# Kernel optimization log

Hardware: AMD Instinct MI355X
Metric: run time of the kernel (lower is better)

Reference implementation:

```python
import jax, jax.numpy as jnp
import numpy as np

B, L, D, H, DK = 2, 1024, 1024, 16, 64
LN_EPS = 1e-5


def setup_inputs() -> dict:
    key = jax.random.key(0)
    ks = jax.random.split(key, 4)
    x = jax.random.normal(ks[0], (B, L, D), dtype=jnp.float32)
    W_qkv = jax.random.normal(ks[1], (D, 3 * D), dtype=jnp.float32) * 0.02
    W_o = jax.random.normal(ks[2], (D, D), dtype=jnp.float32) * 0.02
    W_LTM = jax.random.normal(ks[3], (H, DK, DK), dtype=jnp.float32) * 0.5
    return {
        "x": x,
        "W_qkv": W_qkv,
        "W_o": W_o,
        "W_LTM": W_LTM,
        "V_gs": jnp.zeros((H,), jnp.float32),
        "V_T0": jnp.zeros((H,), jnp.float32),
        "beta_tau": jnp.ones((H,), jnp.float32),
        "beta_gm": jnp.ones((H,), jnp.float32) * 0.1,
        "C_ch": jnp.ones((H,), jnp.float32),
        "gamma": jnp.ones((H,), jnp.float32) * 0.1,
        "alpha_ppd": jnp.ones((1,), jnp.float32),
        "IC_threshold": jnp.ones((1,), jnp.float32),
        "gate": jnp.zeros((H,), jnp.float32),
    }


def _stp_physics(W_LTM, V_gs, V_T0, beta_tau, beta_gm, C_ch, alpha_ppd, IC_threshold):
    # per-head params broadcast to (H, dk, dk)
    V_eff = V_gs[:, None, None] - V_T0[:, None, None] + W_LTM  # U_T = 1.0
    sp = jax.nn.softplus(V_eff)
    g_ch = beta_tau[:, None, None] * sp
    retention = jnp.exp(-g_ch / C_ch[:, None, None])  # = 1 - Lambda
    G = beta_gm[:, None, None] * sp * jax.nn.sigmoid(V_eff)
    sign_mask = jnp.tanh(alpha_ppd * (g_ch - IC_threshold))
    return retention, G, sign_mask


def reference(x, W_qkv, W_o, W_LTM, V_gs, V_T0, beta_tau, beta_gm, C_ch,
              gamma, alpha_ppd, IC_threshold, gate):
    Bb, Ll, Dd = x.shape
    qkv = (x @ W_qkv).reshape(Bb, Ll, 3, H, DK)
    q, k, v = qkv[:, :, 0], qkv[:, :, 1], qkv[:, :, 2]  # (B,L,H,dk)

    # LayerNorm over dk, no affine
    mu = jnp.mean(k, axis=-1, keepdims=True)
    var = jnp.var(k, axis=-1, keepdims=True)
    k_normed = (k - mu) * jax.lax.rsqrt(var + LN_EPS)

    # ---- causal softmax attention ----
    scale = 1.0 / np.sqrt(DK)
    attn = jnp.einsum('bihd,bjhd->bhij', q, k) * scale
    causal = jnp.tril(jnp.ones((Ll, Ll), dtype=bool))
    attn = jnp.where(causal[None, None], attn, -jnp.inf)
    attn = jax.nn.softmax(attn, axis=-1)
    softmax_out = jnp.einsum('bhij,bjhd->bihd', attn, v)  # (B,L,H,dk)

    # ---- STP fast-weight recurrence ----
    retention, G, sign_mask = _stp_physics(W_LTM, V_gs, V_T0, beta_tau,
                                           beta_gm, C_ch, alpha_ppd, IC_threshold)
    coeff = gamma[:, None, None] * sign_mask * G  # (H,dk,dk)

    def step(F_state, qkv_t):
        q_t, k_t, v_t = qkv_t  # (B,H,dk) each; k_t is normed
        hebbian = jnp.einsum('bhd,bhe->bhde', v_t, k_t)
        F_new = retention[None] * F_state + coeff[None] * hebbian
        y_t = jnp.einsum('bhde,bhe->bhd', W_LTM[None] + F_new, q_t)
        return F_new, y_t

    xs = (jnp.moveaxis(q, 1, 0), jnp.moveaxis(k_normed, 1, 0), jnp.moveaxis(v, 1, 0))
    F0 = jnp.zeros((Bb, H, DK, DK), dtype=x.dtype)
    _, ys = jax.lax.scan(step, F0, xs)
    stp_out = jnp.moveaxis(ys, 0, 1)  # (B,L,H,dk)

    g = jax.nn.sigmoid(gate)[None, None, :, None]
    y = g * softmax_out + (1.0 - g) * stp_out
    y = y.reshape(Bb, Ll, Dd)
    return y @ W_o
```

## Files before the change

### kernel.cpp

```cpp
#include <hip/hip_runtime.h>
#include <hip/hip_bf16.h>
#include <math.h>

#define LQ 1024
#define DH 1024
#define NH 16
#define DKH 64

typedef __bf16 bf16x8 __attribute__((ext_vector_type(8)));
typedef float f32x4 __attribute__((ext_vector_type(4)));
typedef const unsigned int __attribute__((address_space(1)))* gas1_t;
typedef unsigned int __attribute__((address_space(3)))* las3_t;

__device__ __forceinline__ unsigned pack2bf(float a, float b) {
  union { __hip_bfloat16 h[2]; unsigned u; } t;
  t.h[0] = __float2bfloat16(a);
  t.h[1] = __float2bfloat16(b);
  return t.u;
}
__device__ __forceinline__ void store_c(float* p, float v) { *p = v; }
__device__ __forceinline__ void store_c(__hip_bfloat16* p, float v) { *p = __float2bfloat16(v); }
__device__ __forceinline__ void bf4w(float* dst, uint2 r) {
  dst[0] = __uint_as_float(r.x << 16);
  dst[1] = __uint_as_float(r.x & 0xffff0000u);
  dst[2] = __uint_as_float(r.y << 16);
  dst[3] = __uint_as_float(r.y & 0xffff0000u);
}

__global__ __launch_bounds__(256) void prep_kernel(
    const float* __restrict__ x, const float* __restrict__ W_qkv, const float* __restrict__ W_o,
    const float* __restrict__ W_LTM, const float* __restrict__ V_gs, const float* __restrict__ V_T0,
    const float* __restrict__ beta_tau, const float* __restrict__ beta_gm, const float* __restrict__ C_ch,
    const float* __restrict__ gamma_, const float* __restrict__ alpha_ppd, const float* __restrict__ IC_thr,
    const float* __restrict__ gate,
    __hip_bfloat16* __restrict__ xb, __hip_bfloat16* __restrict__ wqt, __hip_bfloat16* __restrict__ wot,
    float* __restrict__ ret, float* __restrict__ ret64, float* __restrict__ co, float* __restrict__ g_out) {
  __shared__ float ts[32][33];
  const int bx = blockIdx.x, tid = threadIdx.x;
  if (bx < 256) {
    int idx = bx * 256 + tid;
    int h = idx >> 12;
    float w = W_LTM[idx];
    float veff = V_gs[h] - V_T0[h] + w;
    float sp = fmaxf(veff, 0.f) + log1pf(expf(-fabsf(veff)));
    float gch = beta_tau[h] * sp;
    float e1 = gch / C_ch[h];
    float sig = 1.f / (1.f + expf(-veff));
    float G = beta_gm[h] * sp * sig;
    float sm = tanhf(alpha_ppd[0] * (gch - IC_thr[0]));
    ret[idx] = expf(-e1);
    ret64[idx] = expf(-64.f * e1);
    co[idx] = gamma_[h] * sm * G;
    if (idx < NH) g_out[idx] = 1.f / (1.f + expf(-gate[idx]));
  } else if (bx < 2304) {
    size_t i = (size_t)((bx - 256) * 256 + tid) * 4;
    float4 v = *(const float4*)(x + i);
    __hip_bfloat16 t[4] = {__float2bfloat16(v.x), __float2bfloat16(v.y),
                           __float2bfloat16(v.z), __float2bfloat16(v.w)};
    *(uint2*)(xb + i) = *(uint2*)t;
  } else {
    const float* W;
    __hip_bfloat16* Wt;
    int n0, k0, N;
    if (bx < 5376) {
      int idx = bx - 2304;
      W = W_qkv; Wt = wqt; N = 3072;
      n0 = (idx % 96) * 32; k0 = (idx / 96) * 32;
    } else {
      int idx = bx - 5376;
      W = W_o; Wt = wot; N = 1024;
      n0 = (idx & 31) * 32; k0 = (idx >> 5) * 32;
    }
    int r = tid >> 5, c = tid & 31;
#pragma unroll
    for (int i = 0; i < 4; i++) ts[r + 8 * i][c] = W[(size_t)(k0 + r + 8 * i) * N + n0 + c];
    __syncthreads();
#pragma unroll
    for (int i = 0; i < 4; i++)
      Wt[(size_t)(n0 + r + 8 * i) * 1024 + k0 + c] = __float2bfloat16(ts[c][r + 8 * i]);
  }
}

template <typename OT>
__global__ __launch_bounds__(256) void gemm_bt_kernel(
    const __hip_bfloat16* __restrict__ A, const __hip_bfloat16* __restrict__ Bt,
    OT* __restrict__ C, int M, int N, int K) {
  __shared__ unsigned short As[128 * 32];
  __shared__ unsigned short Bs[128 * 32];
  const int tid = threadIdx.x;
  const int w = tid >> 6, lane = tid & 63;
  const int quad = lane >> 4, l16 = lane & 15;
  const int wm = w & 1, wn = w >> 1;
  const int row0 = blockIdx.y * 128, col0 = blockIdx.x * 128;
  const int sr = lane >> 2;
  const int sk = (lane & 3) * 8;
  f32x4 acc[4][4];
#pragma unroll
  for (int i = 0; i < 4; i++)
#pragma unroll
    for (int j = 0; j < 4; j++) acc[i][j] = (f32x4){0.f, 0.f, 0.f, 0.f};

  for (int k0 = 0; k0 < K; k0 += 32) {
    __syncthreads();
#pragma unroll
    for (int c = 0; c < 2; c++) {
      int s = c * 4 + w;
      const __hip_bfloat16* gA = A + (size_t)(row0 + s * 16 + sr) * K + k0 + sk;
      __builtin_amdgcn_global_load_lds((gas1_t)gA, (las3_t)((char*)As + s * 1024), 16, 0, 0);
      const __hip_bfloat16* gB = Bt + (size_t)(col0 + s * 16 + sr) * K + k0 + sk;
      __builtin_amdgcn_global_load_lds((gas1_t)gB, (las3_t)((char*)Bs + s * 1024), 16, 0, 0);
    }
    __syncthreads();
    bf16x8 af[4], bfr[4];
#pragma unroll
    for (int i = 0; i < 4; i++)
      af[i] = *(const bf16x8*)((const char*)As + (((wm * 64 + i * 16 + l16) * 32 + quad * 8) << 1));
#pragma unroll
    for (int j = 0; j < 4; j++)
      bfr[j] = *(const bf16x8*)((const char*)Bs + (((wn * 64 + j * 16 + l16) * 32 + quad * 8) << 1));
#pragma unroll
    for (int i = 0; i < 4; i++)
#pragma unroll
      for (int j = 0; j < 4; j++)
        acc[i][j] = __builtin_amdgcn_mfma_f32_16x16x32_bf16(af[i], bfr[j], acc[i][j], 0, 0, 0);
  }
#pragma unroll
  for (int i = 0; i < 4; i++) {
    int rowb = row0 + wm * 64 + i * 16 + quad * 4;
#pragma unroll
    for (int j = 0; j < 4; j++) {
      int col = col0 + wn * 64 + j * 16 + l16;
#pragma unroll
      for (int r = 0; r < 4; r++)
        store_c(&C[(size_t)(rowb + r) * N + col], acc[i][j][r]);
    }
  }
}

__global__ __launch_bounds__(256) void cvt_qkv_kernel(
    const __hip_bfloat16* __restrict__ qkvb, __hip_bfloat16* __restrict__ vt,
    __hip_bfloat16* __restrict__ knb) {
  const int tc = blockIdx.x, h = blockIdx.y, b = blockIdx.z;
  const int bh = b * NH + h;
  const int tid = threadIdx.x;
  const int r = tid >> 2;
  const int q4 = tid & 3;
  const int t = tc * 64 + r;
  __shared__ float Ls[64][65];
  const size_t rowbase = (size_t)(b * LQ + t) * 3 * DH + h * DKH + q4 * 16;

  {
    bf16x8 k0 = *(const bf16x8*)(qkvb + rowbase + DH);
    bf16x8 k1 = *(const bf16x8*)(qkvb + rowbase + DH + 8);
    float vv[16];
#pragma unroll
    for (int i = 0; i < 8; i++) { vv[i] = (float)k0[i]; vv[8 + i] = (float)k1[i]; }
    float s1 = 0.f, s2 = 0.f;
#pragma unroll
    for (int i = 0; i < 16; i++) { s1 += vv[i]; s2 += vv[i] * vv[i]; }
    s1 += __shfl_xor(s1, 1); s2 += __shfl_xor(s2, 1);
    s1 += __shfl_xor(s1, 2); s2 += __shfl_xor(s2, 2);
    float mu = s1 * (1.f / 64.f);
    float var = s2 * (1.f / 64.f) - mu * mu;
    float inv = rsqrtf(var + 1e-5f);
    __hip_bfloat16 ko[16];
#pragma unroll
    for (int i = 0; i < 16; i++) ko[i] = __float2bfloat16((vv[i] - mu) * inv);
    __hip_bfloat16* kdst = knb + ((size_t)(b * LQ + t) * NH + h) * DKH + q4 * 16;
    *(uint4*)kdst = *(uint4*)ko;
    *(uint4*)(kdst + 8) = *(uint4*)(ko + 8);
  }
  {
    bf16x8 v0 = *(const bf16x8*)(qkvb + rowbase + 2 * DH);
    bf16x8 v1 = *(const bf16x8*)(qkvb + rowbase + 2 * DH + 8);
#pragma unroll
    for (int i = 0; i < 8; i++) {
      Ls[r][q4 * 16 + i] = (float)v0[i];
      Ls[r][q4 * 16 + 8 + i] = (float)v1[i];
    }
  }
  __syncthreads();
  {
    const int dr = tid >> 2, tq = tid & 3;
    __hip_bfloat16 o[16];
#pragma unroll
    for (int i = 0; i < 16; i++) o[i] = __float2bfloat16(Ls[tq * 16 + i][dr]);
    __hip_bfloat16* dst = vt + ((size_t)bh * DKH + dr) * LQ + tc * 64 + tq * 16;
    *(uint4*)dst = *(uint4*)o;
    *(uint4*)(dst + 8) = *(uint4*)(o + 8);
  }
}

__global__ __launch_bounds__(256) void attn_mfma_kernel(
    const __hip_bfloat16* __restrict__ qkvb, const __hip_bfloat16* __restrict__ vt,
    __hip_bfloat16* __restrict__ sob) {
  const int it = 15 - blockIdx.x;
  const int h = blockIdx.y, b = blockIdx.z;
  const int bh = b * NH + h;
  const int tid = threadIdx.x;
  const int w = tid >> 6, lane = tid & 63;
  const int l16 = lane & 15, quad = lane >> 4;
  __shared__ __attribute__((aligned(16))) __hip_bfloat16 Ks[8 * 64 * 8];
  __shared__ __attribute__((aligned(16))) __hip_bfloat16 Vs[8 * 64 * 8];
  const int i0 = it * 64;
  const int q_abs = i0 + w * 16 + l16;
  bf16x8 aq[2];
  aq[0] = *(const bf16x8*)(qkvb + (size_t)(b * LQ + q_abs) * 3 * DH + h * DKH + quad * 8);
  aq[1] = *(const bf16x8*)(qkvb + (size_t)(b * LQ + q_abs) * 3 * DH + h * DKH + 32 + quad * 8);
  f32x4 o[4];
#pragma unroll
  for (int dt = 0; dt < 4; dt++) o[dt] = (f32x4){0.f, 0.f, 0.f, 0.f};
  float mrun = -3e38f, lrun = 0.f;

  for (int jt = 0; jt <= it; jt++) {
    const int j0 = jt * 64;
    __syncthreads();
#pragma unroll
    for (int ff = 0; ff < 2; ff++) {
      const int f = w * 2 + ff;
      const int nt = f >> 1, kk = f & 1;
      const __hip_bfloat16* gk = qkvb + (size_t)(b * LQ + j0 + nt * 16 + l16) * 3 * DH + DH +
                                 h * DKH + kk * 32 + quad * 8;
      __builtin_amdgcn_global_load_lds((gas1_t)gk, (las3_t)(Ks + f * 512), 16, 0, 0);
      const __hip_bfloat16* gv = vt + ((size_t)bh * DKH + nt * 16 + l16) * LQ + j0 + kk * 32 + quad * 8;
      __builtin_amdgcn_global_load_lds((gas1_t)gv, (las3_t)(Vs + f * 512), 16, 0, 0);
    }
    __syncthreads();
    f32x4 s[4];
#pragma unroll
    for (int nt = 0; nt < 4; nt++) s[nt] = (f32x4){0.f, 0.f, 0.f, 0.f};
#pragma unroll
    for (int kk = 0; kk < 2; kk++)
#pragma unroll
      for (int nt = 0; nt < 4; nt++) {
        bf16x8 bk = *(const bf16x8*)(Ks + ((nt * 2 + kk) * 64 + lane) * 8);
        s[nt] = __builtin_amdgcn_mfma_f32_16x16x32_bf16(bk, aq[kk], s[nt], 0, 0, 0);
      }
#pragma unroll
    for (int nt = 0; nt < 4; nt++)
#pragma unroll
      for (int r = 0; r < 4; r++) {
        float sv = s[nt][r] * 0.125f;
        if (jt == it && (j0 + nt * 16 + quad * 4 + r > q_abs)) sv = -1e30f;
        s[nt][r] = sv;
      }
    float mx = -3e38f;
#pragma unroll
    for (int nt = 0; nt < 4; nt++)
#pragma unroll
      for (int r = 0; r < 4; r++) mx = fmaxf(mx, s[nt][r]);
    mx = fmaxf(mx, __shfl_xor(mx, 16));
    mx = fmaxf(mx, __shfl_xor(mx, 32));
    float mn = fmaxf(mrun, mx);
    float al = __expf(mrun - mn);
    mrun = mn;
    float p[4][4];
    float rs = 0.f;
#pragma unroll
    for (int nt = 0; nt < 4; nt++)
#pragma unroll
      for (int r = 0; r < 4; r++) {
        float pv = __expf(s[nt][r] - mn);
        p[nt][r] = pv;
        rs += pv;
      }
    rs += __shfl_xor(rs, 16);
    rs += __shfl_xor(rs, 32);
    lrun = lrun * al + rs;
    unsigned pk[4][2];
#pragma unroll
    for (int nt = 0; nt < 4; nt++) {
      pk[nt][0] = pack2bf(p[nt][0], p[nt][1]);
      pk[nt][1] = pack2bf(p[nt][2], p[nt][3]);
    }
    const int srcA = l16 | ((quad & 1) << 5);
    const bool hi_sel = (quad >> 1) != 0;
    bf16x8 ap[2];
#pragma unroll
    for (int kk = 0; kk < 2; kk++) {
      union { unsigned u[4]; bf16x8 v; } cv;
#pragma unroll
      for (int g = 0; g < 2; g++) {
        int src = srcA + (g << 4);
        unsigned lo0 = (unsigned)__shfl((int)pk[kk * 2][0], src);
        unsigned lo1 = (unsigned)__shfl((int)pk[kk * 2][1], src);
        unsigned hi0 = (unsigned)__shfl((int)pk[kk * 2 + 1][0], src);
        unsigned hi1 = (unsigned)__shfl((int)pk[kk * 2 + 1][1], src);
        cv.u[g * 2] = hi_sel ? hi0 : lo0;
        cv.u[g * 2 + 1] = hi_sel ? hi1 : lo1;
      }
      ap[kk] = cv.v;
    }
#pragma unroll
    for (int dt = 0; dt < 4; dt++)
#pragma unroll
      for (int r = 0; r < 4; r++) o[dt][r] *= al;
#pragma unroll
    for (int kk = 0; kk < 2; kk++)
#pragma unroll
      for (int dt = 0; dt < 4; dt++) {
        bf16x8 bv = *(const bf16x8*)(Vs + ((dt * 2 + kk) * 64 + lane) * 8);
        o[dt] = __builtin_amdgcn_mfma_f32_16x16x32_bf16(bv, ap[kk], o[dt], 0, 0, 0);
      }
  }
  float inv = 1.f / lrun;
  __hip_bfloat16* ob = sob + ((size_t)(b * LQ + q_abs) * NH + h) * DKH + quad * 4;
#pragma unroll
  for (int dt = 0; dt < 4; dt++) {
    uint2 val = {pack2bf(o[dt][0] * inv, o[dt][1] * inv),
                 pack2bf(o[dt][2] * inv, o[dt][3] * inv)};
    *(uint2*)(ob + dt * 16) = val;
  }
}

__global__ __launch_bounds__(256) void state_kernel(
    const __hip_bfloat16* __restrict__ qkvb, const __hip_bfloat16* __restrict__ knb,
    const float* __restrict__ ret_g, const float* __restrict__ co_g, float* __restrict__ S) {
  const int bh = blockIdx.x >> 1;
  const int half = blockIdx.x & 1;
  const int c = blockIdx.y;
  const int bb = bh >> 4, h = bh & 15;
  const int tid = threadIdx.x;
  const int dl = tid >> 3, j = tid & 7;
  const int d = half * 32 + dl;
  float F[8], R[8], Cc[8];
  const int base = h * 4096 + d * 64 + j * 8;
#pragma unroll
  for (int i = 0; i < 8; i++) {
    F[i] = 0.f;
    R[i] = ret_g[base + i];
    Cc[i] = co_g[base + i];
  }
  __shared__ float kb[2][8][64], vb[2][8][64];
  const int t00 = c * 64;
  const int sten = tid >> 7;
  const int sli = tid & 127;
  const int ss = sli >> 4;
  const int se = (sli & 15) * 4;
  {
    int t = t00 + ss;
    uint2 raw = (sten == 0)
        ? *(const uint2*)(knb + ((size_t)(bb * LQ + t) * NH + h) * DKH + se)
        : *(const uint2*)(qkvb + ((size_t)(bb * LQ + t) * 3 + 2) * DH + h * DKH + se);
    bf4w(sten == 0 ? &kb[0][ss][se] : &vb[0][ss][se], raw);
  }
  __syncthreads();
  for (int sc = 0; sc < 8; sc++) {
    const int p = sc & 1;
    uint2 raw;
    if (sc < 7) {
      int t = t00 + (sc + 1) * 8 + ss;
      raw = (sten == 0)
          ? *(const uint2*)(knb + ((size_t)(bb * LQ + t) * NH + h) * DKH + se)
          : *(const uint2*)(qkvb + ((size_t)(bb * LQ + t) * 3 + 2) * DH + h * DKH + se);
    }
#pragma unroll
    for (int s = 0; s < 8; s++) {
      float vd = vb[p][s][d];
      float4 k0 = *(const float4*)&kb[p][s][j * 8];
      float4 k1 = *(const float4*)&kb[p][s][j * 8 + 4];
      float ke[8] = {k0.x, k0.y, k0.z, k0.w, k1.x, k1.y, k1.z, k1.w};
#pragma unroll
      for (int i = 0; i < 8; i++) F[i] = fmaf(Cc[i] * vd, ke[i], R[i] * F[i]);
    }
    if (sc < 7) bf4w(sten == 0 ? &kb[p ^ 1][ss][se] : &vb[p ^ 1][ss][se], raw);
    __syncthreads();
  }
  const size_t sb = ((size_t)c * 2048 + ((size_t)bb * 16 + h) * 64 + d) * 64 + j * 8;
#pragma unroll
  for (int i = 0; i < 8; i++) S[sb + i] = F[i];
}

__global__ __launch_bounds__(256) void combine_kernel(
    const float* __restrict__ S, const float* __restrict__ ret64, float* __restrict__ Fs) {
  int n = blockIdx.x * 256 + threadIdx.x;
  float r64 = ret64[n & 65535];
  float F = 0.f;
  Fs[n] = 0.f;
#pragma unroll
  for (int c = 1; c < 16; c++) {
    F = fmaf(r64, F, S[(size_t)(c - 1) * 131072 + n]);
    Fs[(size_t)c * 131072 + n] = F;
  }
}

__global__ __launch_bounds__(256) void scan_out_kernel(
    const __hip_bfloat16* __restrict__ qkvb, const __hip_bfloat16* __restrict__ knb,
    const float* __restrict__ W_LTM, const float* __restrict__ ret_g, const float* __restrict__ co_g,
    const float* __restrict__ Fs, const __hip_bfloat16* __restrict__ sob,
    const float* __restrict__ g, __hip_bfloat16* __restrict__ mixb) {
  const int bh = blockIdx.x >> 1;
  const int half = blockIdx.x & 1;
  const int c = blockIdx.y;
  const int bb = bh >> 4, h = bh & 15;
  const int tid = threadIdx.x;
  const int dl = tid >> 3, j = tid & 7;
  const int d = half * 32 + dl;
  const float gh = g[h];
  float F[8], R[8], Cc[8], W[8];
  const int base = h * 4096 + d * 64 + j * 8;
  const size_t nbase = (size_t)c * 131072 + (((size_t)bb * 16 + h) * 64 + d) * 64 + j * 8;
#pragma unroll
  for (int i = 0; i < 8; i++) {
    F[i] = Fs[nbase + i];
    R[i] = ret_g[base + i];
    Cc[i] = co_g[base + i];
    W[i] = W_LTM[base + i];
  }
  __shared__ float qb[2][8][64], kb[2][8][64], vb[2][8][64];
  const int t00 = c * 64;
  const int sten = tid >> 7;
  const int sli = tid & 127;
  const int ss = sli >> 4;
  const int se = (sli & 15) * 4;
  const int vs = tid >> 5;
  const int ve = (tid & 31) * 2;
  {
    int t = t00 + ss, tv = t00 + vs;
    uint2 rqk = (sten == 0)
        ? *(const uint2*)(qkvb + (size_t)(bb * LQ + t) * 3 * DH + h * DKH + se)
        : *(const uint2*)(knb + ((size_t)(bb * LQ + t) * NH + h) * DKH + se);
    unsigned rv = *(const unsigned*)(qkvb + ((size_t)(bb * LQ + tv) * 3 + 2) * DH + h * DKH + ve);
    bf4w(sten == 0 ? &qb[0][ss][se] : &kb[0][ss][se], rqk);
    vb[0][vs][ve] = __uint_as_float(rv << 16);
    vb[0][vs][ve + 1] = __uint_as_float(rv & 0xffff0000u);
  }
  __syncthreads();
  for (int sc = 0; sc < 8; sc++) {
    const int p = sc & 1;
    uint2 rqk;
    unsigned rv;
    if (sc < 7) {
      int t = t00 + (sc + 1) * 8 + ss, tv = t00 + (sc + 1) * 8 + vs;
      rqk = (sten == 0)
          ? *(const uint2*)(qkvb + (size_t)(bb * LQ + t) * 3 * DH + h * DKH + se)
          : *(const uint2*)(knb + ((size_t)(bb * LQ + t) * NH + h) * DKH + se);
      rv = *(const unsigned*)(qkvb + ((size_t)(bb * LQ + tv) * 3 + 2) * DH + h * DKH + ve);
    }
    float ykeep = 0.f;
#pragma unroll
    for (int s = 0; s < 8; s++) {
      float vd = vb[p][s][d];
      float4 k0 = *(const float4*)&kb[p][s][j * 8];
      float4 k1 = *(const float4*)&kb[p][s][j * 8 + 4];
      float4 q0 = *(const float4*)&qb[p][s][j * 8];
      float4 q1 = *(const float4*)&qb[p][s][j * 8 + 4];
      float ke[8] = {k0.x, k0.y, k0.z, k0.w, k1.x, k1.y, k1.z, k1.w};
      float qe[8] = {q0.x, q0.y, q0.z, q0.w, q1.x, q1.y, q1.z, q1.w};
      float yp = 0.f;
#pragma unroll
      for (int i = 0; i < 8; i++) {
        F[i] = fmaf(Cc[i] * vd, ke[i], R[i] * F[i]);
        yp = fmaf(W[i] + F[i], qe[i], yp);
      }
      yp += __shfl_xor(yp, 1);
      yp += __shfl_xor(yp, 2);
      yp += __shfl_xor(yp, 4);
      if (j == s) ykeep = yp;
    }
    {
      const size_t oi = ((size_t)(bb * LQ + t00 + sc * 8 + j) * NH + h) * DKH + d;
      float sv = __bfloat162float(sob[oi]);
      mixb[oi] = __float2bfloat16(gh * sv + (1.f - gh) * ykeep);
    }
    if (sc < 7) {
      bf4w(sten == 0 ? &qb[p ^ 1][ss][se] : &kb[p ^ 1][ss][se], rqk);
      vb[p ^ 1][vs][ve] = __uint_as_float(rv << 16);
      vb[p ^ 1][vs][ve + 1] = __uint_as_float(rv & 0xffff0000u);
    }
    __syncthreads();
  }
}

extern "C" void kernel_launch(void* const* d_in, const int* in_sizes, int n_in,
                              void* d_out, int out_size, void* d_ws, size_t ws_size,
                              hipStream_t stream) {
  (void)in_sizes; (void)n_in; (void)out_size; (void)ws_size;
  const float* x        = (const float*)d_in[0];
  const float* W_qkv    = (const float*)d_in[1];
  const float* W_o      = (const float*)d_in[2];
  const float* W_LTM    = (const float*)d_in[3];
  const float* V_gs     = (const float*)d_in[4];
  const float* V_T0     = (const float*)d_in[5];
  const float* beta_tau = (const float*)d_in[6];
  const float* beta_gm  = (const float*)d_in[7];
  const float* C_ch     = (const float*)d_in[8];
  const float* gamma_   = (const float*)d_in[9];
  const float* alpha_p  = (const float*)d_in[10];
  const float* IC_thr   = (const float*)d_in[11];
  const float* gate     = (const float*)d_in[12];

  float* ws  = (float*)d_ws;
  __hip_bfloat16* qkvb = (__hip_bfloat16*)ws;
  __hip_bfloat16* knb  = (__hip_bfloat16*)(ws + 3145728);
  __hip_bfloat16* sob  = (__hip_bfloat16*)(ws + 4194304);
  __hip_bfloat16* mixb = (__hip_bfloat16*)(ws + 5242880);
  __hip_bfloat16* vtb  = (__hip_bfloat16*)(ws + 6291456);
  __hip_bfloat16* xb   = (__hip_bfloat16*)(ws + 7340032);
  __hip_bfloat16* wqt  = (__hip_bfloat16*)(ws + 8388608);
  __hip_bfloat16* wot  = (__hip_bfloat16*)(ws + 9961472);
  float* ret   = ws + 10485760;
  float* ret64 = ret + 65536;
  float* co    = ret64 + 65536;
  float* g     = co + 65536;
  float* Sbuf  = g + 64;
  float* Fs    = Sbuf + 1966080;
  float* out = (float*)d_out;

  prep_kernel<<<6400, 256, 0, stream>>>(x, W_qkv, W_o, W_LTM, V_gs, V_T0, beta_tau, beta_gm,
                                        C_ch, gamma_, alpha_p, IC_thr, gate,
                                        xb, wqt, wot, ret, ret64, co, g);
  gemm_bt_kernel<__hip_bfloat16><<<dim3(24, 16), 256, 0, stream>>>(xb, wqt, qkvb, 2048, 3072, 1024);
  cvt_qkv_kernel<<<dim3(16, 16, 2), 256, 0, stream>>>(qkvb, vtb, knb);
  attn_mfma_kernel<<<dim3(16, 16, 2), 256, 0, stream>>>(qkvb, vtb, sob);
  state_kernel<<<dim3(64, 15), 256, 0, stream>>>(qkvb, knb, ret, co, Sbuf);
  combine_kernel<<<512, 256, 0, stream>>>(Sbuf, ret64, Fs);
  scan_out_kernel<<<dim3(64, 16), 256, 0, stream>>>(qkvb, knb, W_LTM, ret, co, Fs, sob, g, mixb);
  gemm_bt_kernel<float><<<dim3(8, 16), 256, 0, stream>>>(mixb, wot, out, 2048, 1024, 1024);
}
```

Baseline: 218.0 us.

## Fuse K layernorm and V transpose into QKV GEMM epilogue; smaller output GEMM tiles

The separate cvt_qkv kernel is removed. The QKV GEMM epilogue now computes the per-head LayerNorm of K from accumulator registers using cross-lane shuffles, and writes the transposed V through an LDS buffer that is unioned with the GEMM tiles. This saves a kernel launch and a re-read of the K and V sections from global memory, at the cost of extra epilogue work in two thirds of the blocks. Separately, the output projection uses a new 64x64-tile GEMM with 512 blocks instead of 128, to fill more compute units at the cost of less data reuse per block.

```diff
diff --git a/kernel.cpp b/kernel.cpp
--- a/kernel.cpp
+++ b/kernel.cpp
@@ -18,8 +18,10 @@
   t.h[1] = __float2bfloat16(b);
   return t.u;
 }
-__device__ __forceinline__ void store_c(float* p, float v) { *p = v; }
-__device__ __forceinline__ void store_c(__hip_bfloat16* p, float v) { *p = __float2bfloat16(v); }
+__device__ __forceinline__ unsigned short bfbits(float x) {
+  __hip_bfloat16 h = __float2bfloat16(x);
+  return *(unsigned short*)&h;
+}
 __device__ __forceinline__ void bf4w(float* dst, uint2 r) {
   dst[0] = __uint_as_float(r.x << 16);
   dst[1] = __uint_as_float(r.x & 0xffff0000u);
@@ -81,12 +83,14 @@
   }
 }
 
-template <typename OT>
-__global__ __launch_bounds__(256) void gemm_bt_kernel(
+__global__ __launch_bounds__(256) void gemm_qkv_kernel(
     const __hip_bfloat16* __restrict__ A, const __hip_bfloat16* __restrict__ Bt,
-    OT* __restrict__ C, int M, int N, int K) {
-  __shared__ unsigned short As[128 * 32];
-  __shared__ unsigned short Bs[128 * 32];
+    __hip_bfloat16* __restrict__ C, __hip_bfloat16* __restrict__ knb,
+    __hip_bfloat16* __restrict__ vt, int M, int N, int K) {
+  __shared__ union {
+    struct { unsigned short As[128 * 32]; unsigned short Bs[128 * 32]; } ab;
+    unsigned short Vt[4][64][68];
+  } sm;
   const int tid = threadIdx.x;
   const int w = tid >> 6, lane = tid & 63;
   const int quad = lane >> 4, l16 = lane & 15;
@@ -106,18 +110,18 @@
     for (int c = 0; c < 2; c++) {
       int s = c * 4 + w;
       const __hip_bfloat16* gA = A + (size_t)(row0 + s * 16 + sr) * K + k0 + sk;
-      __builtin_amdgcn_global_load_lds((gas1_t)gA, (las3_t)((char*)As + s * 1024), 16, 0, 0);
+      __builtin_amdgcn_global_load_lds((gas1_t)gA, (las3_t)((char*)sm.ab.As + s * 1024), 16, 0, 0);
       const __hip_bfloat16* gB = Bt + (size_t)(col0 + s * 16 + sr) * K + k0 + sk;
-      __builtin_amdgcn_global_load_lds((gas1_t)gB, (las3_t)((char*)Bs + s * 1024), 16, 0, 0);
+      __builtin_amdgcn_global_load_lds((gas1_t)gB, (las3_t)((char*)sm.ab.Bs + s * 1024), 16, 0, 0);
     }
     __syncthreads();
     bf16x8 af[4], bfr[4];
 #pragma unroll
     for (int i = 0; i < 4; i++)
-      af[i] = *(const bf16x8*)((const char*)As + (((wm * 64 + i * 16 + l16) * 32 + quad * 8) << 1));
+      af[i] = *(const bf16x8*)((const char*)sm.ab.As + (((wm * 64 + i * 16 + l16) * 32 + quad * 8) << 1));
 #pragma unroll
     for (int j = 0; j < 4; j++)
-      bfr[j] = *(const bf16x8*)((const char*)Bs + (((wn * 64 + j * 16 + l16) * 32 + quad * 8) << 1));
+      bfr[j] = *(const bf16x8*)((const char*)sm.ab.Bs + (((wn * 64 + j * 16 + l16) * 32 + quad * 8) << 1));
 #pragma unroll
     for (int i = 0; i < 4; i++)
 #pragma unroll
@@ -132,62 +136,113 @@
       int col = col0 + wn * 64 + j * 16 + l16;
 #pragma unroll
       for (int r = 0; r < 4; r++)
-        store_c(&C[(size_t)(rowb + r) * N + col], acc[i][j][r]);
-    }
-  }
-}
-
-__global__ __launch_bounds__(256) void cvt_qkv_kernel(
-    const __hip_bfloat16* __restrict__ qkvb, __hip_bfloat16* __restrict__ vt,
-    __hip_bfloat16* __restrict__ knb) {
-  const int tc = blockIdx.x, h = blockIdx.y, b = blockIdx.z;
-  const int bh = b * NH + h;
+        C[(size_t)(rowb + r) * N + col] = __float2bfloat16(acc[i][j][r]);
+    }
+  }
+  const int sec = col0 >> 10;
+  if (sec == 1) {
+    const int hh = ((col0 & 1023) >> 6) + wn;
+#pragma unroll
+    for (int i = 0; i < 4; i++) {
+      f32x4 s1 = {0.f, 0.f, 0.f, 0.f}, s2 = {0.f, 0.f, 0.f, 0.f};
+#pragma unroll
+      for (int j = 0; j < 4; j++)
+#pragma unroll
+        for (int r = 0; r < 4; r++) {
+          s1[r] += acc[i][j][r];
+          s2[r] += acc[i][j][r] * acc[i][j][r];
+        }
+#pragma unroll
+      for (int m = 1; m <= 8; m <<= 1)
+#pragma unroll
+        for (int r = 0; r < 4; r++) {
+          s1[r] += __shfl_xor(s1[r], m);
+          s2[r] += __shfl_xor(s2[r], m);
+        }
+#pragma unroll
+      for (int r = 0; r < 4; r++) {
+        float mu = s1[r] * (1.f / 64.f);
+        float var = s2[r] * (1.f / 64.f) - mu * mu;
+        float inv = rsqrtf(var + 1e-5f);
+        int row = row0 + wm * 64 + i * 16 + quad * 4 + r;
+#pragma unroll
+        for (int j = 0; j < 4; j++)
+          knb[((size_t)row * NH + hh) * DKH + j * 16 + l16] = __float2bfloat16((acc[i][j][r] - mu) * inv);
+      }
+    }
+  } else if (sec == 2) {
+    __syncthreads();
+    const int hh = ((col0 & 1023) >> 6) + wn;
+#pragma unroll
+    for (int i = 0; i < 4; i++)
+#pragma unroll
+      for (int j = 0; j < 4; j++)
+#pragma unroll
+        for (int r = 0; r < 4; r++)
+          sm.Vt[w][j * 16 + l16][i * 16 + quad * 4 + r] = bfbits(acc[i][j][r]);
+    const int b = row0 >> 10;
+    const int t0 = (row0 & 1023) + wm * 64;
+    const int bh = b * NH + hh;
+    const int cc = lane & 7, ddl = lane >> 3;
+#pragma unroll
+    for (int pass = 0; pass < 8; pass++) {
+      int d = pass * 8 + ddl;
+      uint2 a0 = *(const uint2*)&sm.Vt[w][d][cc * 8];
+      uint2 a1 = *(const uint2*)&sm.Vt[w][d][cc * 8 + 4];
+      uint4 val = {a0.x, a0.y, a1.x, a1.y};
+      *(uint4*)(vt + ((size_t)bh * DKH + d) * LQ + t0 + cc * 8) = val;
+    }
+  }
+}
+
+__global__ __launch_bounds__(256) void gemm_bt64_kernel(
+    const __hip_bfloat16* __restrict__ A, const __hip_bfloat16* __restrict__ Bt,
+    float* __restrict__ C, int M, int N, int K) {
+  __shared__ unsigned short As[64 * 32];
+  __shared__ unsigned short Bs[64 * 32];
   const int tid = threadIdx.x;
-  const int r = tid >> 2;
-  const int q4 = tid & 3;
-  const int t = tc * 64 + r;
-  __shared__ float Ls[64][65];
-  const size_t rowbase = (size_t)(b * LQ + t) * 3 * DH + h * DKH + q4 * 16;
-
-  {
-    bf16x8 k0 = *(const bf16x8*)(qkvb + rowbase + DH);
-    bf16x8 k1 = *(const bf16x8*)(qkvb + rowbase + DH + 8);
-    float vv[16];
-#pragma unroll
-    for (int i = 0; i < 8; i++) { vv[i] = (float)k0[i]; vv[8 + i] = (float)k1[i]; }
-    float s1 = 0.f, s2 = 0.f;
-#pragma unroll
-    for (int i = 0; i < 16; i++) { s1 += vv[i]; s2 += vv[i] * vv[i]; }
-    s1 += __shfl_xor(s1, 1); s2 += __shfl_xor(s2, 1);
-    s1 += __shfl_xor(s1, 2); s2 += __shfl_xor(s2, 2);
-    float mu = s1 * (1.f / 64.f);
-    float var = s2 * (1.f / 64.f) - mu * mu;
-    float inv = rsqrtf(var + 1e-5f);
-    __hip_bfloat16 ko[16];
-#pragma unroll
-    for (int i = 0; i < 16; i++) ko[i] = __float2bfloat16((vv[i] - mu) * inv);
-    __hip_bfloat16* kdst = knb + ((size_t)(b * LQ + t) * NH + h) * DKH + q4 * 16;
-    *(uint4*)kdst = *(uint4*)ko;
-    *(uint4*)(kdst + 8) = *(uint4*)(ko + 8);
-  }
-  {
-    bf16x8 v0 = *(const bf16x8*)(qkvb + rowbase + 2 * DH);
-    bf16x8 v1 = *(const bf16x8*)(qkvb + rowbase + 2 * DH + 8);
-#pragma unroll
-    for (int i = 0; i < 8; i++) {
-      Ls[r][q4 * 16 + i] = (float)v0[i];
-      Ls[r][q4 * 16 + 8 + i] = (float)v1[i];
-    }
-  }
-  __syncthreads();
-  {
-    const int dr = tid >> 2, tq = tid & 3;
-    __hip_bfloat16 o[16];
-#pragma unroll
-    for (int i = 0; i < 16; i++) o[i] = __float2bfloat16(Ls[tq * 16 + i][dr]);
-    __hip_bfloat16* dst = vt + ((size_t)bh * DKH + dr) * LQ + tc * 64 + tq * 16;
-    *(uint4*)dst = *(uint4*)o;
-    *(uint4*)(dst + 8) = *(uint4*)(o + 8);
+  const int w = tid >> 6, lane = tid & 63;
+  const int quad = lane >> 4, l16 = lane & 15;
+  const int wm = w & 1, wn = w >> 1;
+  const int row0 = blockIdx.y * 64, col0 = blockIdx.x * 64;
+  const int sr = lane >> 2;
+  const int sk = (lane & 3) * 8;
+  f32x4 acc[2][2];
+#pragma unroll
+  for (int i = 0; i < 2; i++)
+#pragma unroll
+    for (int j = 0; j < 2; j++) acc[i][j] = (f32x4){0.f, 0.f, 0.f, 0.f};
+
+  for (int k0 = 0; k0 < K; k0 += 32) {
+    __syncthreads();
+    const __hip_bfloat16* gA = A + (size_t)(row0 + w * 16 + sr) * K + k0 + sk;
+    __builtin_amdgcn_global_load_lds((gas1_t)gA, (las3_t)((char*)As + w * 1024), 16, 0, 0);
+    const __hip_bfloat16* gB = Bt + (size_t)(col0 + w * 16 + sr) * K + k0 + sk;
+    __builtin_amdgcn_global_load_lds((gas1_t)gB, (las3_t)((char*)Bs + w * 1024), 16, 0, 0);
+    __syncthreads();
+    bf16x8 af[2], bfr[2];
+#pragma unroll
+    for (int i = 0; i < 2; i++)
+      af[i] = *(const bf16x8*)((const char*)As + (((wm * 32 + i * 16 + l16) * 32 + quad * 8) << 1));
+#pragma unroll
+    for (int j = 0; j < 2; j++)
+      bfr[j] = *(const bf16x8*)((const char*)Bs + (((wn * 32 + j * 16 + l16) * 32 + quad * 8) << 1));
+#pragma unroll
+    for (int i = 0; i < 2; i++)
+#pragma unroll
+      for (int j = 0; j < 2; j++)
+        acc[i][j] = __builtin_amdgcn_mfma_f32_16x16x32_bf16(af[i], bfr[j], acc[i][j], 0, 0, 0);
+  }
+#pragma unroll
+  for (int i = 0; i < 2; i++) {
+    int rowb = row0 + wm * 32 + i * 16 + quad * 4;
+#pragma unroll
+    for (int j = 0; j < 2; j++) {
+      int col = col0 + wn * 32 + j * 16 + l16;
+#pragma unroll
+      for (int r = 0; r < 4; r++)
+        C[(size_t)(rowb + r) * N + col] = acc[i][j][r];
+    }
   }
 }
 
@@ -510,11 +565,10 @@
   prep_kernel<<<6400, 256, 0, stream>>>(x, W_qkv, W_o, W_LTM, V_gs, V_T0, beta_tau, beta_gm,
                                         C_ch, gamma_, alpha_p, IC_thr, gate,
                                         xb, wqt, wot, ret, ret64, co, g);
-  gemm_bt_kernel<__hip_bfloat16><<<dim3(24, 16), 256, 0, stream>>>(xb, wqt, qkvb, 2048, 3072, 1024);
-  cvt_qkv_kernel<<<dim3(16, 16, 2), 256, 0, stream>>>(qkvb, vtb, knb);
+  gemm_qkv_kernel<<<dim3(24, 16), 256, 0, stream>>>(xb, wqt, qkvb, knb, vtb, 2048, 3072, 1024);
   attn_mfma_kernel<<<dim3(16, 16, 2), 256, 0, stream>>>(qkvb, vtb, sob);
   state_kernel<<<dim3(64, 15), 256, 0, stream>>>(qkvb, knb, ret, co, Sbuf);
   combine_kernel<<<512, 256, 0, stream>>>(Sbuf, ret64, Fs);
   scan_out_kernel<<<dim3(64, 16), 256, 0, stream>>>(qkvb, knb, W_LTM, ret, co, Fs, sob, g, mixb);
-  gemm_bt_kernel<float><<<dim3(8, 16), 256, 0, stream>>>(mixb, wot, out, 2048, 1024, 1024);
-}
+  gemm_bt64_kernel<<<dim3(16, 32), 256, 0, stream>>>(mixb, wot, out, 2048, 1024, 1024);
+}
```

Result: no change. 214.9 us (-1.4%).
